# Performance work log

Measured on AMD Instinct MI355X. Metric: run time of the kernel, lower is better.

Reference implementation:

```python
import jax, jax.numpy as jnp
import numpy as np

N_NODES = 100000
N_EDGES = 1200000
HIDDEN = 64
EDGE_DIM = 16
LN_EPS = 1e-6  # flax LayerNorm default


def setup_inputs() -> dict:
    key = jax.random.key(0)
    ks = jax.random.split(key, 10)
    node_features = jax.random.normal(ks[0], (N_NODES, HIDDEN), dtype=jnp.float32)
    edge_index = jax.random.randint(ks[1], (2, N_EDGES), 0, N_NODES, dtype=jnp.int64)
    edge_features = jax.random.normal(ks[2], (N_EDGES, EDGE_DIM), dtype=jnp.float32)
    # Dense(hidden) on concat([src_feat, edge_features]) -> in = HIDDEN+EDGE_DIM
    s1 = 1.0 / np.sqrt(HIDDEN + EDGE_DIM)
    W1 = jax.random.normal(ks[3], (HIDDEN + EDGE_DIM, HIDDEN), dtype=jnp.float32) * s1
    b1 = jnp.zeros((HIDDEN,), dtype=jnp.float32)
    s2 = 1.0 / np.sqrt(HIDDEN)
    W2 = jax.random.normal(ks[4], (HIDDEN, HIDDEN), dtype=jnp.float32) * s2
    b2 = jnp.zeros((HIDDEN,), dtype=jnp.float32)
    # update Dense on concat([node_features, agg]) -> in = 2*HIDDEN
    s3 = 1.0 / np.sqrt(2 * HIDDEN)
    W3 = jax.random.normal(ks[5], (2 * HIDDEN, HIDDEN), dtype=jnp.float32) * s3
    b3 = jnp.zeros((HIDDEN,), dtype=jnp.float32)
    ln_scale = jnp.ones((HIDDEN,), dtype=jnp.float32)
    ln_bias = jnp.zeros((HIDDEN,), dtype=jnp.float32)
    return {
        "node_features": node_features,
        "edge_features": edge_features,
        "edge_index": edge_index,
        "W1": W1, "b1": b1, "W2": W2, "b2": b2,
        "W3": W3, "b3": b3,
        "ln_scale": ln_scale, "ln_bias": ln_bias,
    }


def reference(node_features, edge_features, edge_index, W1, b1, W2, b2, W3, b3, ln_scale, ln_bias):
    # eval mode: dropout is identity (deterministic)
    src, dst = edge_index[0], edge_index[1]
    src_feat = node_features[src]                                  # [E, H] gather
    msg = jnp.concatenate([src_feat, edge_features], axis=-1)      # [E, H+Fe]
    msg = jax.nn.gelu(msg @ W1 + b1)                               # [E, H]
    msg = msg @ W2 + b2                                            # [E, H]
    agg = jax.ops.segment_sum(msg, dst, num_segments=node_features.shape[0])  # [N, H]
    upd = jnp.concatenate([node_features, agg], axis=-1)           # [N, 2H]
    h = upd @ W3 + b3                                              # [N, H]
    # LayerNorm (flax default: eps=1e-6, with scale and bias)
    mu = jnp.mean(h, axis=-1, keepdims=True)
    var = jnp.mean(jnp.square(h - mu), axis=-1, keepdims=True)
    h = (h - mu) * jax.lax.rsqrt(var + LN_EPS) * ln_scale + ln_bias
    h = jax.nn.gelu(h)
    # residual (node feature dim == hidden_dim)
    return h + node_features
```

## Files before the change

### kernel.cpp

```cpp
#include <hip/hip_runtime.h>

#define TE 64
#define TN 64

union F4 { float4 v; float f[4]; };

__device__ __forceinline__ float gelu_f(float x) {
    const float c0 = 0.7978845608028654f;
    float z = c0 * (x + 0.044715f * x * x * x);
    float ez = __builtin_exp2f(z * 2.8853900817779268f);
    float th = 1.0f - 2.0f * __builtin_amdgcn_rcpf(ez + 1.0f);
    return 0.5f * x * (1.0f + th);
}

__device__ __forceinline__ void barrier_lgkm() {
    asm volatile("s_waitcnt lgkmcnt(0)" ::: "memory");
    __builtin_amdgcn_s_barrier();
}

__global__ __launch_bounds__(256, 4) void edge_mlp_kernel(
    const float* __restrict__ nf,
    const float* __restrict__ ef,
    const int*   __restrict__ ei,
    const int*   __restrict__ eids,
    const int2*  __restrict__ sd,
    const float* __restrict__ np,
    const float* __restrict__ W1,
    const float* __restrict__ b1,
    const float* __restrict__ W2,
    const float* __restrict__ b2,
    float*       agg,
    int nE, int nTiles)
{
    __shared__ float sX[80][TE + 4];
    __shared__ float sM[64][TE + 4];
    __shared__ int   sDst[TE];
    __shared__ int   sSrc[TE];

    const int t    = threadIdx.x;
    const int lane = t & 63;
    const int w    = t >> 6;
    const int e0   = (t & 15) * 4;
    const int c0   = (t >> 4) * 4;
    const bool sorted = (eids != nullptr);
    const bool useNP  = (np != nullptr);
    F4 b1v;
    b1v.v = *(const float4*)(b1 + c0);

    for (int tile = blockIdx.x; tile < nTiles; tile += gridDim.x) {
        const int gbase = tile * TE;
        {
            const int idx = gbase + lane;
            const int ci = idx < nE ? idx : nE - 1;
            int ge, src, dstv;
            if (sorted) {
                ge = eids[ci];
                const int2 p = sd[ci];
                src  = p.x;
                dstv = (idx < nE) ? p.y : -1;
            } else {
                ge   = ci;
                src  = ei[ge];
                dstv = (idx < nE) ? ei[nE + ge] : -1;
            }
            F4 ev;
            ev.v = *(const float4*)(ef + (size_t)ge * 16 + w * 4);
            if (useNP) {
                #pragma unroll
                for (int j = 0; j < 4; ++j)
                    sX[w * 4 + j][lane] = ev.f[j];
            } else {
                const float4* nrow = (const float4*)(nf + (size_t)src * 64);
                F4 a0, a1, a2, a3;
                a0.v = nrow[w * 4 + 0];
                a1.v = nrow[w * 4 + 1];
                a2.v = nrow[w * 4 + 2];
                a3.v = nrow[w * 4 + 3];
                const int kb = w * 16;
                #pragma unroll
                for (int j = 0; j < 4; ++j) {
                    sX[kb + 0  + j][lane] = a0.f[j];
                    sX[kb + 4  + j][lane] = a1.f[j];
                    sX[kb + 8  + j][lane] = a2.f[j];
                    sX[kb + 12 + j][lane] = a3.f[j];
                    sX[64 + w * 4 + j][lane] = ev.f[j];
                }
            }
            if (w == 0) sDst[lane] = dstv;
            if (w == 1) sSrc[lane] = src;
        }
        barrier_lgkm();

        float acc[4][4] = {};
        if (useNP) {
            #pragma unroll
            for (int k = 0; k < 16; ++k) {
                F4 xv, wv;
                xv.v = *(const float4*)&sX[k][e0];
                wv.v = *(const float4*)(W1 + (64 + k) * 64 + c0);
                #pragma unroll
                for (int i = 0; i < 4; ++i)
                    #pragma unroll
                    for (int j = 0; j < 4; ++j)
                        acc[i][j] = fmaf(xv.f[i], wv.f[j], acc[i][j]);
            }
            #pragma unroll
            for (int i = 0; i < 4; ++i) {
                F4 npv;
                npv.v = *(const float4*)(np + (size_t)sSrc[e0 + i] * 64 + c0);
                #pragma unroll
                for (int j = 0; j < 4; ++j)
                    acc[i][j] += npv.f[j];
            }
        } else {
            #pragma unroll 8
            for (int k = 0; k < 80; ++k) {
                F4 xv, wv;
                xv.v = *(const float4*)&sX[k][e0];
                wv.v = *(const float4*)(W1 + k * 64 + c0);
                #pragma unroll
                for (int i = 0; i < 4; ++i)
                    #pragma unroll
                    for (int j = 0; j < 4; ++j)
                        acc[i][j] = fmaf(xv.f[i], wv.f[j], acc[i][j]);
            }
        }

        #pragma unroll
        for (int j = 0; j < 4; ++j) {
            F4 col;
            #pragma unroll
            for (int i = 0; i < 4; ++i)
                col.f[i] = gelu_f(acc[i][j] + b1v.f[j]);
            *(float4*)&sM[c0 + j][e0] = col.v;
        }
        barrier_lgkm();

        if (sorted) {
            const int c  = t >> 2;
            const int q  = t & 3;
            const int cb = q * 16;
            int   cur = -1;
            float run = 0.f;
            #pragma unroll
            for (int s = 0; s < 4; ++s) {
                F4 rv;
                rv.v = *(const float4*)&sM[c][cb + s * 4];
                #pragma unroll
                for (int j = 0; j < 4; ++j) {
                    const int d = sDst[cb + s * 4 + j];
                    if (d != cur) {
                        if (cur >= 0)
                            __hip_atomic_fetch_add(agg + (size_t)cur * 64 + c, run,
                                                   __ATOMIC_RELAXED, __HIP_MEMORY_SCOPE_AGENT);
                        cur = d;
                        run = 0.f;
                    }
                    if (d >= 0) run += rv.f[j];
                }
            }
            if (cur >= 0)
                __hip_atomic_fetch_add(agg + (size_t)cur * 64 + c, run,
                                       __ATOMIC_RELAXED, __HIP_MEMORY_SCOPE_AGENT);
            barrier_lgkm();
        } else {
            float acc2[4][4] = {};
            #pragma unroll 8
            for (int k = 0; k < 64; ++k) {
                F4 xv, wv;
                xv.v = *(const float4*)&sM[k][e0];
                wv.v = *(const float4*)(W2 + k * 64 + c0);
                #pragma unroll
                for (int i = 0; i < 4; ++i)
                    #pragma unroll
                    for (int j = 0; j < 4; ++j)
                        acc2[i][j] = fmaf(xv.f[i], wv.f[j], acc2[i][j]);
            }
            F4 b2v;
            b2v.v = *(const float4*)(b2 + c0);
            #pragma unroll
            for (int i = 0; i < 4; ++i) {
                if (gbase + e0 + i < nE) {
                    float* arow = agg + (size_t)sDst[e0 + i] * 64 + c0;
                    #pragma unroll
                    for (int j = 0; j < 4; ++j)
                        __hip_atomic_fetch_add(arow + j, acc2[i][j] + b2v.f[j],
                                               __ATOMIC_RELAXED, __HIP_MEMORY_SCOPE_AGENT);
                }
            }
            barrier_lgkm();
        }
    }
}

__global__ __launch_bounds__(256) void node_part_kernel(
    const float* __restrict__ nf, const float* __restrict__ W1,
    float* __restrict__ np, int nN)
{
    __shared__ float sU[64][TN + 4];
    const int t = threadIdx.x;
    const int lane = t & 63;
    const int w = t >> 6;
    const int tb = blockIdx.x * TN;
    const int node = (tb + lane < nN) ? tb + lane : nN - 1;
    {
        const float4* nrow = (const float4*)(nf + (size_t)node * 64);
        F4 a0, a1, a2, a3;
        a0.v = nrow[w * 4 + 0];
        a1.v = nrow[w * 4 + 1];
        a2.v = nrow[w * 4 + 2];
        a3.v = nrow[w * 4 + 3];
        const int kb = w * 16;
        #pragma unroll
        for (int j = 0; j < 4; ++j) {
            sU[kb + 0  + j][lane] = a0.f[j];
            sU[kb + 4  + j][lane] = a1.f[j];
            sU[kb + 8  + j][lane] = a2.f[j];
            sU[kb + 12 + j][lane] = a3.f[j];
        }
    }
    barrier_lgkm();
    const int n0 = (t & 15) * 4;
    const int c0 = (t >> 4) * 4;
    float acc[4][4] = {};
    #pragma unroll 8
    for (int k = 0; k < 64; ++k) {
        F4 xv, wv;
        xv.v = *(const float4*)&sU[k][n0];
        wv.v = *(const float4*)(W1 + k * 64 + c0);
        #pragma unroll
        for (int i = 0; i < 4; ++i)
            #pragma unroll
            for (int j = 0; j < 4; ++j)
                acc[i][j] = fmaf(xv.f[i], wv.f[j], acc[i][j]);
    }
    #pragma unroll
    for (int i = 0; i < 4; ++i) {
        const int gnode = tb + n0 + i;
        if (gnode < nN) {
            F4 o;
            #pragma unroll
            for (int j = 0; j < 4; ++j) o.f[j] = acc[i][j];
            *(float4*)(np + (size_t)gnode * 64 + c0) = o.v;
        }
    }
}

__global__ void prep_w23_kernel(const float* __restrict__ W2, const float* __restrict__ W3,
                                const float* __restrict__ b2,
                                float* __restrict__ W23, float* __restrict__ b2w)
{
    const int t = threadIdx.x;
    const int c = t & 63;
    const int kg = t >> 6;
    for (int k = kg * 16; k < kg * 16 + 16; ++k) {
        float s = 0.f;
        for (int m = 0; m < 64; ++m)
            s = fmaf(W2[k * 64 + m], W3[(64 + m) * 64 + c], s);
        W23[k * 64 + c] = s;
    }
    if (t < 64) {
        float s = 0.f;
        for (int m = 0; m < 64; ++m)
            s = fmaf(b2[m], W3[(64 + m) * 64 + t], s);
        b2w[t] = s;
    }
}

__global__ __launch_bounds__(256) void hist_kernel(const int* __restrict__ dst,
                                                   int* __restrict__ counts, int nE) {
    int e = blockIdx.x * 256 + threadIdx.x;
    const int stride = gridDim.x * 256;
    for (; e < nE; e += stride)
        atomicAdd(&counts[dst[e]], 1);
}

__global__ __launch_bounds__(256) void scan_local_kernel(const int* __restrict__ in,
                                                         int* __restrict__ out,
                                                         int* __restrict__ bsum, int n) {
    __shared__ int s[256];
    const int t = threadIdx.x;
    const int base = blockIdx.x * 2048 + t * 8;
    int v[8];
    #pragma unroll
    for (int i = 0; i < 8; ++i) v[i] = (base + i < n) ? in[base + i] : 0;
    int run = 0;
    #pragma unroll
    for (int i = 0; i < 8; ++i) { int c = v[i]; v[i] = run; run += c; }
    s[t] = run;
    __syncthreads();
    int x = run;
    for (int off = 1; off < 256; off <<= 1) {
        int y = (t >= off) ? s[t - off] : 0;
        __syncthreads();
        x += y; s[t] = x;
        __syncthreads();
    }
    const int texcl = x - run;
    if (t == 255) bsum[blockIdx.x] = x;
    #pragma unroll
    for (int i = 0; i < 8; ++i)
        if (base + i < n) out[base + i] = texcl + v[i];
}

__global__ void scan_bsums_kernel(int* bsum, int nb) {
    const int l = threadIdx.x;
    if (nb <= 64) {
        int v = (l < nb) ? bsum[l] : 0;
        const int orig = v;
        for (int off = 1; off < 64; off <<= 1) {
            int y = __shfl_up(v, off, 64);
            if (l >= off) v += y;
        }
        if (l < nb) bsum[l] = v - orig;
    } else if (l == 0) {
        int run = 0;
        for (int b = 0; b < nb; ++b) { int tt = bsum[b]; bsum[b] = run; run += tt; }
    }
}

__global__ __launch_bounds__(256) void scan_add_kernel(int* __restrict__ offs,
                                                       const int* __restrict__ bsum,
                                                       int* __restrict__ cursor, int n) {
    const int base = blockIdx.x * 2048 + threadIdx.x * 8;
    const int add = bsum[blockIdx.x];
    #pragma unroll
    for (int i = 0; i < 8; ++i)
        if (base + i < n) { int v = offs[base + i] + add; offs[base + i] = v; cursor[base + i] = v; }
}

__global__ __launch_bounds__(256) void scatter_kernel(const int* __restrict__ ei,
                                                      int* __restrict__ cursor,
                                                      int* __restrict__ eids,
                                                      int2* __restrict__ sd, int nE) {
    int e = blockIdx.x * 256 + threadIdx.x;
    const int stride = gridDim.x * 256;
    for (; e < nE; e += stride) {
        const int s = ei[e];
        const int d = ei[nE + e];
        const int pos = atomicAdd(&cursor[d], 1);
        eids[pos] = e;
        sd[pos] = make_int2(s, d);
    }
}

__global__ __launch_bounds__(256) void node_update_kernel(
    const float* __restrict__ nf,
    const float* gsum,
    const float* __restrict__ W3,
    const float* __restrict__ wB,
    const float* __restrict__ b3,
    const float* __restrict__ cvec,
    const int*   __restrict__ counts,
    const float* __restrict__ lns,
    const float* __restrict__ lnb,
    float* out, int nN)
{
    __shared__ float sW3[128][64];
    __shared__ float sU[128][TN + 4];
    __shared__ float sP1[16][TN];
    __shared__ float sP2[16][TN];
    __shared__ float sMu[TN];
    __shared__ float sRs[TN];

    const int t = threadIdx.x;
    for (int i = t * 4; i < 64 * 64; i += 1024)
        *(float4*)((float*)sW3 + i) = *(const float4*)(W3 + i);
    for (int i = t * 4; i < 64 * 64; i += 1024)
        *(float4*)((float*)sW3 + 4096 + i) = *(const float4*)(wB + i);

    const int lane = t & 63;
    const int w    = t >> 6;
    const int tb   = blockIdx.x * TN;
    const int node = tb + lane;
    const bool valid = node < nN;

    {
        const float* base = (w < 2) ? (nf   + (size_t)node * 64 + w * 32)
                                    : (gsum + (size_t)node * 64 + (w - 2) * 32);
        const int kb = (w < 2) ? (w * 32) : (64 + (w - 2) * 32);
        #pragma unroll
        for (int q = 0; q < 8; ++q) {
            F4 v;
            v.v = valid ? *(const float4*)(base + q * 4) : make_float4(0.f, 0.f, 0.f, 0.f);
            #pragma unroll
            for (int j = 0; j < 4; ++j)
                sU[kb + q * 4 + j][lane] = v.f[j];
        }
    }

    const int n0 = (t & 15) * 4;
    const int c0 = (t >> 4) * 4;
    F4 b3v, sv, bv, cv;
    b3v.v = *(const float4*)(b3  + c0);
    sv.v  = *(const float4*)(lns + c0);
    bv.v  = *(const float4*)(lnb + c0);
    if (cvec) cv.v = *(const float4*)(cvec + c0);
    __syncthreads();

    float acc[4][4] = {};
    #pragma unroll 8
    for (int k = 0; k < 128; ++k) {
        F4 xv, wv;
        xv.v = *(const float4*)&sU[k][n0];
        wv.v = *(const float4*)&sW3[k][c0];
        #pragma unroll
        for (int i = 0; i < 4; ++i)
            #pragma unroll
            for (int j = 0; j < 4; ++j)
                acc[i][j] = fmaf(xv.f[i], wv.f[j], acc[i][j]);
    }

    float h[4][4];
    #pragma unroll
    for (int i = 0; i < 4; ++i) {
        float cf = 0.f;
        if (counts) {
            const int gnode = tb + n0 + i;
            cf = (float)counts[gnode < nN ? gnode : nN - 1];
        }
        #pragma unroll
        for (int j = 0; j < 4; ++j) {
            float v = acc[i][j] + b3v.f[j];
            if (cvec) v = fmaf(cf, cv.f[j], v);
            h[i][j] = v;
        }
    }

    const int cg = t >> 4;
    #pragma unroll
    for (int i = 0; i < 4; ++i) {
        float s1 = h[i][0] + h[i][1] + h[i][2] + h[i][3];
        float s2 = h[i][0]*h[i][0] + h[i][1]*h[i][1] + h[i][2]*h[i][2] + h[i][3]*h[i][3];
        sP1[cg][n0 + i] = s1;
        sP2[cg][n0 + i] = s2;
    }
    __syncthreads();
    if (t < TN) {
        float m1 = 0.f, m2 = 0.f;
        #pragma unroll
        for (int g = 0; g < 16; ++g) { m1 += sP1[g][t]; m2 += sP2[g][t]; }
        float mu  = m1 * (1.f / 64.f);
        float var = m2 * (1.f / 64.f) - mu * mu;
        sMu[t] = mu;
        sRs[t] = rsqrtf(var + 1e-6f);
    }
    __syncthreads();

    #pragma unroll
    for (int i = 0; i < 4; ++i) {
        const int gnode = tb + n0 + i;
        const float mu = sMu[n0 + i];
        const float rs = sRs[n0 + i];
        if (gnode < nN) {
            #pragma unroll
            for (int j = 0; j < 4; ++j) {
                float xn = (h[i][j] - mu) * rs * sv.f[j] + bv.f[j];
                float r  = gelu_f(xn) + sU[c0 + j][n0 + i];
                out[(size_t)gnode * 64 + c0 + j] = r;
            }
        }
    }
}

extern "C" void kernel_launch(void* const* d_in, const int* in_sizes, int n_in,
                              void* d_out, int out_size, void* d_ws, size_t ws_size,
                              hipStream_t stream)
{
    const float* nf  = (const float*)d_in[0];
    const float* ef  = (const float*)d_in[1];
    const int*   ei  = (const int*)  d_in[2];
    const float* W1  = (const float*)d_in[3];
    const float* b1  = (const float*)d_in[4];
    const float* W2  = (const float*)d_in[5];
    const float* b2  = (const float*)d_in[6];
    const float* W3  = (const float*)d_in[7];
    const float* b3  = (const float*)d_in[8];
    const float* lns = (const float*)d_in[9];
    const float* lnb = (const float*)d_in[10];

    const int nN = in_sizes[0] / 64;
    const int nE = in_sizes[2] / 2;
    float* out = (float*)d_out;
    const int* dstArr = ei + nE;

    const int nTiles = (nE + TE - 1) / TE;
    const int gridA  = nTiles < 1024 ? nTiles : 1024;
    const int gridB  = (nN + TN - 1) / TN;

    char* ws = (char*)d_ws;
    size_t off = 0;
    auto take = [&](size_t bytes) { void* p = ws + off; off = (off + bytes + 255) & ~(size_t)255; return p; };
    int*   counts = (int*)  take((size_t)nN * 4);
    int*   offs   = (int*)  take((size_t)nN * 4);
    int*   cursor = (int*)  take((size_t)nN * 4);
    int*   bsum   = (int*)  take(4096);
    int*   eids   = (int*)  take((size_t)nE * 4);
    int2*  sd     = (int2*) take((size_t)nE * 8);
    float* W23    = (float*)take(64 * 64 * 4);
    float* b2w    = (float*)take(64 * 4);
    const size_t tier1End = off;
    float* npart  = (float*)take((size_t)nN * 64 * 4);
    const size_t tier2End = off;
    float* gsumw  = (float*)take((size_t)nN * 64 * 4);
    const size_t tier3End = off;
    const size_t aggBytes = (size_t)nN * 64 * 4;

    if (ws_size >= tier1End) {
        const bool useNP = (ws_size >= tier2End);
        float* gsum = (ws_size >= tier3End) ? gsumw : out;
        const int nb = (nN + 2047) / 2048;
        hipMemsetAsync(counts, 0, (size_t)nN * 4, stream);
        hipMemsetAsync(gsum, 0, aggBytes, stream);
        hipLaunchKernelGGL(hist_kernel, dim3(2048), dim3(256), 0, stream, dstArr, counts, nE);
        hipLaunchKernelGGL(scan_local_kernel, dim3(nb), dim3(256), 0, stream, counts, offs, bsum, nN);
        hipLaunchKernelGGL(scan_bsums_kernel, dim3(1), dim3(64), 0, stream, bsum, nb);
        hipLaunchKernelGGL(scan_add_kernel, dim3(nb), dim3(256), 0, stream, offs, bsum, cursor, nN);
        hipLaunchKernelGGL(scatter_kernel, dim3(2048), dim3(256), 0, stream, ei, cursor, eids, sd, nE);
        hipLaunchKernelGGL(prep_w23_kernel, dim3(1), dim3(256), 0, stream, W2, W3, b2, W23, b2w);
        if (useNP)
            hipLaunchKernelGGL(node_part_kernel, dim3(gridB), dim3(256), 0, stream, nf, W1, npart, nN);
        hipLaunchKernelGGL(edge_mlp_kernel, dim3(gridA), dim3(256), 0, stream,
                           nf, ef, ei, eids, sd, useNP ? npart : (const float*)nullptr,
                           W1, b1, W2, b2, gsum, nE, nTiles);
        hipLaunchKernelGGL(node_update_kernel, dim3(gridB), dim3(256), 0, stream,
                           nf, gsum, W3, W23, b3, b2w, counts, lns, lnb, out, nN);
    } else {
        float* agg = (ws_size >= aggBytes) ? (float*)d_ws : out;
        hipMemsetAsync(agg, 0, aggBytes, stream);
        hipLaunchKernelGGL(edge_mlp_kernel, dim3(gridA), dim3(256), 0, stream,
                           nf, ef, ei, (const int*)nullptr, (const int2*)nullptr, (const float*)nullptr,
                           W1, b1, W2, b2, agg, nE, nTiles);
        hipLaunchKernelGGL(node_update_kernel, dim3(gridB), dim3(256), 0, stream,
                           nf, agg, W3, W3 + 64 * 64, b3, (const float*)nullptr, (const int*)nullptr,
                           lns, lnb, out, nN);
    }
}
```

Baseline: 427.3 us.

## Replace tiled edge kernel with per-wavefront contiguous-run edge kernel for sorted path

```diff
diff --git a/kernel.cpp b/kernel.cpp
--- a/kernel.cpp
+++ b/kernel.cpp
@@ -18,114 +18,134 @@
     __builtin_amdgcn_s_barrier();
 }
 
-__global__ __launch_bounds__(256, 4) void edge_mlp_kernel(
-    const float* __restrict__ nf,
+__global__ __launch_bounds__(256, 8) void edge_run_kernel(
     const float* __restrict__ ef,
-    const int*   __restrict__ ei,
     const int*   __restrict__ eids,
     const int2*  __restrict__ sd,
     const float* __restrict__ np,
     const float* __restrict__ W1,
     const float* __restrict__ b1,
-    const float* __restrict__ W2,
-    const float* __restrict__ b2,
-    float*       agg,
-    int nE, int nTiles)
+    float*       __restrict__ gsum,
+    int nE, int epw)
+{
+    const int lane = threadIdx.x & 63;
+    const int wgid = blockIdx.x * 4 + (threadIdx.x >> 6);
+    const int r0 = wgid * epw;
+    if (r0 >= nE) return;
+    const int r1 = (r0 + epw < nE) ? r0 + epw : nE;
+
+    float W1p[16];
+    #pragma unroll
+    for (int k = 0; k < 16; ++k)
+        W1p[k] = W1[(64 + k) * 64 + lane];
+    const float b1v = b1[lane];
+
+    int   cur = -1;
+    float run = 0.f;
+
+    for (int e = r0; e < r1; e += 4) {
+        const int li  = lane & 3;
+        const int idx = (e + li < nE) ? e + li : nE - 1;
+        const int  eid4 = eids[idx];
+        const int2 sd2  = sd[idx];
+        const int  ge   = __shfl(eid4, lane >> 4);
+        const float efv = ef[(size_t)ge * 16 + (lane & 15)];
+
+        int srcj[4], dstj[4];
+        #pragma unroll
+        for (int j = 0; j < 4; ++j) {
+            srcj[j] = __shfl(sd2.x, j);
+            dstj[j] = __shfl(sd2.y, j);
+        }
+        float npv[4];
+        #pragma unroll
+        for (int j = 0; j < 4; ++j)
+            npv[j] = np[(size_t)srcj[j] * 64 + lane];
+
+        #pragma unroll
+        for (int j = 0; j < 4; ++j) {
+            if (e + j < r1) {
+                float acc = npv[j];
+                #pragma unroll
+                for (int k = 0; k < 16; ++k)
+                    acc = fmaf(__shfl(efv, j * 16 + k), W1p[k], acc);
+                const float g = gelu_f(acc + b1v);
+                const int d = dstj[j];
+                if (d != cur) {
+                    if (cur >= 0)
+                        __hip_atomic_fetch_add(gsum + (size_t)cur * 64 + lane, run,
+                                               __ATOMIC_RELAXED, __HIP_MEMORY_SCOPE_AGENT);
+                    cur = d;
+                    run = 0.f;
+                }
+                run += g;
+            }
+        }
+    }
+    if (cur >= 0)
+        __hip_atomic_fetch_add(gsum + (size_t)cur * 64 + lane, run,
+                               __ATOMIC_RELAXED, __HIP_MEMORY_SCOPE_AGENT);
+}
+
+__global__ __launch_bounds__(256, 4) void edge_mlp_kernel(
+    const float* __restrict__ nf, const float* __restrict__ ef,
+    const int* __restrict__ ei,
+    const float* __restrict__ W1, const float* __restrict__ b1,
+    const float* __restrict__ W2, const float* __restrict__ b2,
+    float* agg, int nE, int nTiles)
 {
     __shared__ float sX[80][TE + 4];
     __shared__ float sM[64][TE + 4];
     __shared__ int   sDst[TE];
-    __shared__ int   sSrc[TE];
 
     const int t    = threadIdx.x;
     const int lane = t & 63;
     const int w    = t >> 6;
     const int e0   = (t & 15) * 4;
     const int c0   = (t >> 4) * 4;
-    const bool sorted = (eids != nullptr);
-    const bool useNP  = (np != nullptr);
-    F4 b1v;
+    F4 b1v, b2v;
     b1v.v = *(const float4*)(b1 + c0);
+    b2v.v = *(const float4*)(b2 + c0);
 
     for (int tile = blockIdx.x; tile < nTiles; tile += gridDim.x) {
         const int gbase = tile * TE;
         {
             const int idx = gbase + lane;
-            const int ci = idx < nE ? idx : nE - 1;
-            int ge, src, dstv;
-            if (sorted) {
-                ge = eids[ci];
-                const int2 p = sd[ci];
-                src  = p.x;
-                dstv = (idx < nE) ? p.y : -1;
-            } else {
-                ge   = ci;
-                src  = ei[ge];
-                dstv = (idx < nE) ? ei[nE + ge] : -1;
+            const int ge  = idx < nE ? idx : nE - 1;
+            const int src = ei[ge];
+            const int dstv = (idx < nE) ? ei[nE + ge] : -1;
+            const float4* nrow = (const float4*)(nf + (size_t)src * 64);
+            F4 a0, a1, a2, a3, ev;
+            a0.v = nrow[w * 4 + 0];
+            a1.v = nrow[w * 4 + 1];
+            a2.v = nrow[w * 4 + 2];
+            a3.v = nrow[w * 4 + 3];
+            ev.v = *(const float4*)(ef + (size_t)ge * 16 + w * 4);
+            const int kb = w * 16;
+            #pragma unroll
+            for (int j = 0; j < 4; ++j) {
+                sX[kb + 0  + j][lane] = a0.f[j];
+                sX[kb + 4  + j][lane] = a1.f[j];
+                sX[kb + 8  + j][lane] = a2.f[j];
+                sX[kb + 12 + j][lane] = a3.f[j];
+                sX[64 + w * 4 + j][lane] = ev.f[j];
             }
-            F4 ev;
-            ev.v = *(const float4*)(ef + (size_t)ge * 16 + w * 4);
-            if (useNP) {
+            if (w == 0) sDst[lane] = dstv;
+        }
+        barrier_lgkm();
+
+        float acc[4][4] = {};
+        #pragma unroll 8
+        for (int k = 0; k < 80; ++k) {
+            F4 xv, wv;
+            xv.v = *(const float4*)&sX[k][e0];
+            wv.v = *(const float4*)(W1 + k * 64 + c0);
+            #pragma unroll
+            for (int i = 0; i < 4; ++i)
                 #pragma unroll
                 for (int j = 0; j < 4; ++j)
-                    sX[w * 4 + j][lane] = ev.f[j];
-            } else {
-                const float4* nrow = (const float4*)(nf + (size_t)src * 64);
-                F4 a0, a1, a2, a3;
-                a0.v = nrow[w * 4 + 0];
-                a1.v = nrow[w * 4 + 1];
-                a2.v = nrow[w * 4 + 2];
-                a3.v = nrow[w * 4 + 3];
-                const int kb = w * 16;
-                #pragma unroll
-                for (int j = 0; j < 4; ++j) {
-                    sX[kb + 0  + j][lane] = a0.f[j];
-                    sX[kb + 4  + j][lane] = a1.f[j];
-                    sX[kb + 8  + j][lane] = a2.f[j];
-                    sX[kb + 12 + j][lane] = a3.f[j];
-                    sX[64 + w * 4 + j][lane] = ev.f[j];
-                }
-            }
-            if (w == 0) sDst[lane] = dstv;
-            if (w == 1) sSrc[lane] = src;
-        }
-        barrier_lgkm();
-
-        float acc[4][4] = {};
-        if (useNP) {
-            #pragma unroll
-            for (int k = 0; k < 16; ++k) {
-                F4 xv, wv;
-                xv.v = *(const float4*)&sX[k][e0];
-                wv.v = *(const float4*)(W1 + (64 + k) * 64 + c0);
-                #pragma unroll
-                for (int i = 0; i < 4; ++i)
-                    #pragma unroll
-                    for (int j = 0; j < 4; ++j)
-                        acc[i][j] = fmaf(xv.f[i], wv.f[j], acc[i][j]);
-            }
-            #pragma unroll
-            for (int i = 0; i < 4; ++i) {
-                F4 npv;
-                npv.v = *(const float4*)(np + (size_t)sSrc[e0 + i] * 64 + c0);
-                #pragma unroll
-                for (int j = 0; j < 4; ++j)
-                    acc[i][j] += npv.f[j];
-            }
-        } else {
-            #pragma unroll 8
-            for (int k = 0; k < 80; ++k) {
-                F4 xv, wv;
-                xv.v = *(const float4*)&sX[k][e0];
-                wv.v = *(const float4*)(W1 + k * 64 + c0);
-                #pragma unroll
-                for (int i = 0; i < 4; ++i)
-                    #pragma unroll
-                    for (int j = 0; j < 4; ++j)
-                        acc[i][j] = fmaf(xv.f[i], wv.f[j], acc[i][j]);
-            }
-        }
-
+                    acc[i][j] = fmaf(xv.f[i], wv.f[j], acc[i][j]);
+        }
         #pragma unroll
         for (int j = 0; j < 4; ++j) {
             F4 col;
@@ -136,60 +156,29 @@
         }
         barrier_lgkm();
 
-        if (sorted) {
-            const int c  = t >> 2;
-            const int q  = t & 3;
-            const int cb = q * 16;
-            int   cur = -1;
-            float run = 0.f;
-            #pragma unroll
-            for (int s = 0; s < 4; ++s) {
-                F4 rv;
-                rv.v = *(const float4*)&sM[c][cb + s * 4];
+        float acc2[4][4] = {};
+        #pragma unroll 8
+        for (int k = 0; k < 64; ++k) {
+            F4 xv, wv;
+            xv.v = *(const float4*)&sM[k][e0];
+            wv.v = *(const float4*)(W2 + k * 64 + c0);
+            #pragma unroll
+            for (int i = 0; i < 4; ++i)
                 #pragma unroll
-                for (int j = 0; j < 4; ++j) {
-                    const int d = sDst[cb + s * 4 + j];
-                    if (d != cur) {
-                        if (cur >= 0)
-                            __hip_atomic_fetch_add(agg + (size_t)cur * 64 + c, run,
-                                                   __ATOMIC_RELAXED, __HIP_MEMORY_SCOPE_AGENT);
-                        cur = d;
-                        run = 0.f;
-                    }
-                    if (d >= 0) run += rv.f[j];
-                }
+                for (int j = 0; j < 4; ++j)
+                    acc2[i][j] = fmaf(xv.f[i], wv.f[j], acc2[i][j]);
+        }
+        #pragma unroll
+        for (int i = 0; i < 4; ++i) {
+            if (gbase + e0 + i < nE) {
+                float* arow = agg + (size_t)sDst[e0 + i] * 64 + c0;
+                #pragma unroll
+                for (int j = 0; j < 4; ++j)
+                    __hip_atomic_fetch_add(arow + j, acc2[i][j] + b2v.f[j],
+                                           __ATOMIC_RELAXED, __HIP_MEMORY_SCOPE_AGENT);
             }
-            if (cur >= 0)
-                __hip_atomic_fetch_add(agg + (size_t)cur * 64 + c, run,
-                                       __ATOMIC_RELAXED, __HIP_MEMORY_SCOPE_AGENT);
-            barrier_lgkm();
-        } else {
-            float acc2[4][4] = {};
-            #pragma unroll 8
-            for (int k = 0; k < 64; ++k) {
-                F4 xv, wv;
-                xv.v = *(const float4*)&sM[k][e0];
-                wv.v = *(const float4*)(W2 + k * 64 + c0);
-                #pragma unroll
-                for (int i = 0; i < 4; ++i)
-                    #pragma unroll
-                    for (int j = 0; j < 4; ++j)
-                        acc2[i][j] = fmaf(xv.f[i], wv.f[j], acc2[i][j]);
-            }
-            F4 b2v;
-            b2v.v = *(const float4*)(b2 + c0);
-            #pragma unroll
-            for (int i = 0; i < 4; ++i) {
-                if (gbase + e0 + i < nE) {
-                    float* arow = agg + (size_t)sDst[e0 + i] * 64 + c0;
-                    #pragma unroll
-                    for (int j = 0; j < 4; ++j)
-                        __hip_atomic_fetch_add(arow + j, acc2[i][j] + b2v.f[j],
-                                               __ATOMIC_RELAXED, __HIP_MEMORY_SCOPE_AGENT);
-                }
-            }
-            barrier_lgkm();
-        }
+        }
+        barrier_lgkm();
     }
 }
 
@@ -484,9 +473,7 @@
     float* out = (float*)d_out;
     const int* dstArr = ei + nE;
 
-    const int nTiles = (nE + TE - 1) / TE;
-    const int gridA  = nTiles < 1024 ? nTiles : 1024;
-    const int gridB  = (nN + TN - 1) / TN;
+    const int gridB = (nN + TN - 1) / TN;
 
     char* ws = (char*)d_ws;
     size_t off = 0;
@@ -499,15 +486,13 @@
     int2*  sd     = (int2*) take((size_t)nE * 8);
     float* W23    = (float*)take(64 * 64 * 4);
     float* b2w    = (float*)take(64 * 4);
-    const size_t tier1End = off;
     float* npart  = (float*)take((size_t)nN * 64 * 4);
     const size_t tier2End = off;
     float* gsumw  = (float*)take((size_t)nN * 64 * 4);
     const size_t tier3End = off;
     const size_t aggBytes = (size_t)nN * 64 * 4;
 
-    if (ws_size >= tier1End) {
-        const bool useNP = (ws_size >= tier2End);
+    if (ws_size >= tier2End) {
         float* gsum = (ws_size >= tier3End) ? gsumw : out;
         const int nb = (nN + 2047) / 2048;
         hipMemsetAsync(counts, 0, (size_t)nN * 4, stream);
@@ -518,19 +503,22 @@
         hipLaunchKernelGGL(scan_add_kernel, dim3(nb), dim3(256), 0, stream, offs, bsum, cursor, nN);
         hipLaunchKernelGGL(scatter_kernel, dim3(2048), dim3(256), 0, stream, ei, cursor, eids, sd, nE);
         hipLaunchKernelGGL(prep_w23_kernel, dim3(1), dim3(256), 0, stream, W2, W3, b2, W23, b2w);
-        if (useNP)
-            hipLaunchKernelGGL(node_part_kernel, dim3(gridB), dim3(256), 0, stream, nf, W1, npart, nN);
-        hipLaunchKernelGGL(edge_mlp_kernel, dim3(gridA), dim3(256), 0, stream,
-                           nf, ef, ei, eids, sd, useNP ? npart : (const float*)nullptr,
-                           W1, b1, W2, b2, gsum, nE, nTiles);
+        hipLaunchKernelGGL(node_part_kernel, dim3(gridB), dim3(256), 0, stream, nf, W1, npart, nN);
+
+        const int gridE = 2048;
+        const int epw   = (nE + gridE * 4 - 1) / (gridE * 4);
+        hipLaunchKernelGGL(edge_run_kernel, dim3(gridE), dim3(256), 0, stream,
+                           ef, eids, sd, npart, W1, b1, gsum, nE, epw);
+
         hipLaunchKernelGGL(node_update_kernel, dim3(gridB), dim3(256), 0, stream,
                            nf, gsum, W3, W23, b3, b2w, counts, lns, lnb, out, nN);
     } else {
+        const int nTiles = (nE + TE - 1) / TE;
+        const int gridA  = nTiles < 1024 ? nTiles : 1024;
         float* agg = (ws_size >= aggBytes) ? (float*)d_ws : out;
         hipMemsetAsync(agg, 0, aggBytes, stream);
         hipLaunchKernelGGL(edge_mlp_kernel, dim3(gridA), dim3(256), 0, stream,
-                           nf, ef, ei, (const int*)nullptr, (const int2*)nullptr, (const float*)nullptr,
-                           W1, b1, W2, b2, agg, nE, nTiles);
+                           nf, ef, ei, W1, b1, W2, b2, agg, nE, nTiles);
         hipLaunchKernelGGL(node_update_kernel, dim3(gridB), dim3(256), 0, stream,
                            nf, agg, W3, W3 + 64 * 64, b3, (const float*)nullptr, (const int*)nullptr,
                            lns, lnb, out, nN);
```

Result: slower. 480.7 us (+12.5%).
